# Optimization experiments

Hardware: AMD Instinct MI355X
Metric: run time of the kernel (lower is better)

## Reference

```python
import jax, jax.numpy as jnp
import numpy as np

D_EMB, D_PROJ, N_HEADS, HIDDEN = 640, 256, 4, 128
HEAD_DIM = D_PROJ // N_HEADS
B = 65536
EPS = 1e-5


def setup_inputs() -> dict:
    key = jax.random.key(0)
    ks = jax.random.split(key, 14)
    def w(k, shape, fan_in):
        return (jax.random.normal(k, shape, jnp.float32) / np.sqrt(fan_in)).astype(jnp.float32)
    return {
        "global_diff": jax.random.normal(ks[0], (B, D_EMB), jnp.float32),
        "local_diff": jax.random.normal(ks[1], (B, D_EMB), jnp.float32),
        # global/local projections ([in, out] layout; math identical to torch Linear)
        "Wg": w(ks[2], (D_EMB, D_PROJ), D_EMB), "bg": jnp.zeros((D_PROJ,), jnp.float32),
        "Wl": w(ks[3], (D_EMB, D_PROJ), D_EMB), "bl": jnp.zeros((D_PROJ,), jnp.float32),
        # MultiheadAttention packed in-proj (q|k|v) and out-proj
        "W_in": w(ks[4], (D_PROJ, 3 * D_PROJ), D_PROJ), "b_in": jnp.zeros((3 * D_PROJ,), jnp.float32),
        "W_out": w(ks[5], (D_PROJ, D_PROJ), D_PROJ), "b_out": jnp.zeros((D_PROJ,), jnp.float32),
        # LayerNorm
        "gamma": jnp.ones((D_PROJ,), jnp.float32), "beta": jnp.zeros((D_PROJ,), jnp.float32),
        # MLP head
        "W1": w(ks[6], (D_PROJ, HIDDEN), D_PROJ), "b1": jnp.zeros((HIDDEN,), jnp.float32),
        "W2": w(ks[7], (HIDDEN, 1), HIDDEN), "b2": jnp.zeros((1,), jnp.float32),
    }


def reference(global_diff, local_diff, Wg, bg, Wl, bl, W_in, b_in, W_out, b_out,
              gamma, beta, W1, b1, W2, b2):
    # projections (eval mode: dropout inactive)
    g = global_diff @ Wg + bg              # [B, P] -- the single query token
    l = local_diff @ Wl + bl               # [B, P]
    kv = jnp.stack([g, l], axis=1)         # [B, 2, P]

    Wq, Wk, Wv = jnp.split(W_in, 3, axis=1)
    bq, bk, bv = jnp.split(b_in, 3)
    b = g.shape[0]
    q = (g @ Wq + bq).reshape(b, N_HEADS, HEAD_DIM)        # [B, H, d]
    k = (kv @ Wk + bk).reshape(b, 2, N_HEADS, HEAD_DIM)    # [B, 2, H, d]
    v = (kv @ Wv + bv).reshape(b, 2, N_HEADS, HEAD_DIM)

    scale = 1.0 / np.sqrt(HEAD_DIM)
    scores = jnp.einsum('bhd,bshd->bhs', q, k) * scale     # [B, H, 2]
    attn = jax.nn.softmax(scores, axis=-1)
    ctx = jnp.einsum('bhs,bshd->bhd', attn, v).reshape(b, D_PROJ)
    attended = ctx @ W_out + b_out                         # [B, P]

    # residual + LayerNorm (eps=1e-5, torch default)
    x = g + attended
    mu = jnp.mean(x, axis=-1, keepdims=True)
    var = jnp.mean(jnp.square(x - mu), axis=-1, keepdims=True)
    y = (x - mu) * jax.lax.rsqrt(var + EPS) * gamma + beta

    # MLP head: Linear -> exact GELU (torch default) -> Linear
    h = jax.nn.gelu(y @ W1 + b1, approximate=False)
    out = (h @ W2 + b2).squeeze(-1)                        # [B]
    return out
```

## Files before the change

kernel.cpp:

```cpp
#include <hip/hip_runtime.h>
#include <math.h>

typedef __attribute__((ext_vector_type(4))) float f32x4;
typedef __attribute__((ext_vector_type(8))) __bf16 bf16x8;

static constexpr int WG_OFF = 0;
static constexpr int WL_OFF = 163840;
static constexpr int WQ_OFF = 327680;
static constexpr int WK_OFF = 393216;
static constexpr int WV_OFF = 458752;
static constexpr int WO_OFF = 524288;
static constexpr int W1_OFF = 589824;
static constexpr int W_TOTAL = 622592;

__device__ __forceinline__ unsigned short f2bf(float f) {
  unsigned u = __builtin_bit_cast(unsigned, f);
  u += 0x7FFFu + ((u >> 16) & 1u);
  return (unsigned short)(u >> 16);
}

__device__ __forceinline__ f32x4 mfma16(bf16x8 a, bf16x8 b, f32x4 c) {
  return __builtin_amdgcn_mfma_f32_16x16x32_bf16(a, b, c, 0, 0, 0);
}
__device__ __forceinline__ f32x4 fzero4() {
  f32x4 v; v[0] = 0.f; v[1] = 0.f; v[2] = 0.f; v[3] = 0.f; return v;
}

__device__ __forceinline__ bf16x8 ldB(const unsigned short* __restrict__ ws, int fragIdx, int lane) {
  return *(const bf16x8*)(ws + (size_t)(fragIdx * 64 + lane) * 8);
}

template <int STRIDE>
__device__ __forceinline__ bf16x8 ldA(const char* s, int row, int kbyte) {
  return *(const bf16x8*)(s + row * STRIDE + (kbyte ^ ((row & 7) << 4)));
}

__device__ __forceinline__ void stC(char* s, int row, int col, float v) {
  *(__bf16*)(s + row * 512 + ((col * 2) ^ ((row & 7) << 4))) = (__bf16)v;
}
__device__ __forceinline__ float ldC(const char* s, int row, int col) {
  return (float)*(const __bf16*)(s + row * 512 + ((col * 2) ^ ((row & 7) << 4)));
}

__device__ __forceinline__ bf16x8 cvt8(float4 a, float4 b) {
  bf16x8 t;
  t[0] = (__bf16)a.x; t[1] = (__bf16)a.y; t[2] = (__bf16)a.z; t[3] = (__bf16)a.w;
  t[4] = (__bf16)b.x; t[5] = (__bf16)b.y; t[6] = (__bf16)b.z; t[7] = (__bf16)b.w;
  return t;
}

template <int N>
__device__ __forceinline__ void red16(float* v) {
#pragma unroll
  for (int m = 1; m < 16; m <<= 1) {
#pragma unroll
    for (int i = 0; i < N; ++i) v[i] += __shfl_xor(v[i], m);
  }
}

__device__ __forceinline__ void stageA32(const float* __restrict__ A, char* sA, int tid) {
#pragma unroll
  for (int i = 0; i < 5; ++i) {
    const int idx = i * 512 + tid;
    const int row = idx / 80;
    const int c8 = idx - row * 80;
    const float* ap = A + (size_t)idx * 8;
    float4 f0 = *(const float4*)ap;
    float4 f1 = *(const float4*)(ap + 4);
    *(bf16x8*)(sA + row * 1280 + ((c8 * 16) ^ ((row & 7) << 4))) = cvt8(f0, f1);
  }
}

__device__ __forceinline__ void proj640(const char* sA, const unsigned short* __restrict__ wsW,
                                        const float* __restrict__ bias, char* sDst,
                                        int f0, int lane) {
  const int l15 = lane & 15, kg4 = lane >> 4;
  f32x4 acc[2][2];
#pragma unroll
  for (int m = 0; m < 2; ++m)
#pragma unroll
    for (int n = 0; n < 2; ++n) acc[m][n] = fzero4();
#pragma unroll 2
  for (int kt = 0; kt < 20; ++kt) {
    bf16x8 b0 = ldB(wsW, kt * 16 + f0, lane);
    bf16x8 b1 = ldB(wsW, kt * 16 + f0 + 1, lane);
    const int kb = kt * 64 + kg4 * 16;
#pragma unroll
    for (int m = 0; m < 2; ++m) {
      bf16x8 a = ldA<1280>(sA, m * 16 + l15, kb);
      acc[m][0] = mfma16(a, b0, acc[m][0]);
      acc[m][1] = mfma16(a, b1, acc[m][1]);
    }
  }
#pragma unroll
  for (int n = 0; n < 2; ++n) {
    const int col = (f0 + n) * 16 + l15;
    const float bv = bias[col];
#pragma unroll
    for (int m = 0; m < 2; ++m)
#pragma unroll
      for (int r = 0; r < 4; ++r)
        stC(sDst, m * 16 + kg4 * 4 + r, col, acc[m][n][r] + bv);
  }
}

__device__ __forceinline__ void gemm256(const char* sA, const unsigned short* __restrict__ wsW,
                                        int f0, f32x4 (&acc)[2][2], int lane) {
  const int l15 = lane & 15, kg4 = lane >> 4;
#pragma unroll 2
  for (int kt = 0; kt < 8; ++kt) {
    bf16x8 b0 = ldB(wsW, kt * 16 + f0, lane);
    bf16x8 b1 = ldB(wsW, kt * 16 + f0 + 1, lane);
    const int kb = kt * 64 + kg4 * 16;
#pragma unroll
    for (int m = 0; m < 2; ++m) {
      bf16x8 a = ldA<512>(sA, m * 16 + l15, kb);
      acc[m][0] = mfma16(a, b0, acc[m][0]);
      acc[m][1] = mfma16(a, b1, acc[m][1]);
    }
  }
}

__device__ __forceinline__ void gemm256d(const char* sG, const char* sL,
                                         const unsigned short* __restrict__ wsW, int f0,
                                         f32x4 (&ag)[2][2], f32x4 (&al)[2][2], int lane) {
  const int l15 = lane & 15, kg4 = lane >> 4;
#pragma unroll 2
  for (int kt = 0; kt < 8; ++kt) {
    bf16x8 b0 = ldB(wsW, kt * 16 + f0, lane);
    bf16x8 b1 = ldB(wsW, kt * 16 + f0 + 1, lane);
    const int kb = kt * 64 + kg4 * 16;
#pragma unroll
    for (int m = 0; m < 2; ++m) {
      bf16x8 g = ldA<512>(sG, m * 16 + l15, kb);
      bf16x8 l = ldA<512>(sL, m * 16 + l15, kb);
      ag[m][0] = mfma16(g, b0, ag[m][0]);
      ag[m][1] = mfma16(g, b1, ag[m][1]);
      al[m][0] = mfma16(l, b0, al[m][0]);
      al[m][1] = mfma16(l, b1, al[m][1]);
    }
  }
}

__global__ void convert_w(const float* __restrict__ Wg, const float* __restrict__ Wl,
                          const float* __restrict__ Win, const float* __restrict__ Wout,
                          const float* __restrict__ W1, unsigned short* __restrict__ ws) {
  const int tid = blockIdx.x * 256 + threadIdx.x;
  if (tid >= W_TOTAL) return;
  const float* src;
  int stride, coloff, base, lognf;
  if (tid < WL_OFF)      { src = Wg;   stride = 256; coloff = 0;   base = WG_OFF; lognf = 4; }
  else if (tid < WQ_OFF) { src = Wl;   stride = 256; coloff = 0;   base = WL_OFF; lognf = 4; }
  else if (tid < WK_OFF) { src = Win;  stride = 768; coloff = 0;   base = WQ_OFF; lognf = 4; }
  else if (tid < WV_OFF) { src = Win;  stride = 768; coloff = 256; base = WK_OFF; lognf = 4; }
  else if (tid < WO_OFF) { src = Win;  stride = 768; coloff = 512; base = WV_OFF; lognf = 4; }
  else if (tid < W1_OFF) { src = Wout; stride = 256; coloff = 0;   base = WO_OFF; lognf = 4; }
  else                   { src = W1;   stride = 128; coloff = 0;   base = W1_OFF; lognf = 3; }
  const int idx = tid - base;
  const int j = idx & 7;
  const int lane = (idx >> 3) & 63;
  const int fl = idx >> 9;
  const int n = fl & ((1 << lognf) - 1);
  const int kt = fl >> lognf;
  const int k = kt * 32 + (lane >> 4) * 8 + j;
  const int col = coloff + n * 16 + (lane & 15);
  ws[tid] = f2bf(src[k * stride + col]);
}

__global__ __launch_bounds__(512)
__attribute__((amdgpu_waves_per_eu(4, 4)))
void dca_fused(
    const float* __restrict__ gdiff, const float* __restrict__ ldiff,
    const float* __restrict__ bg, const float* __restrict__ bl,
    const float* __restrict__ bin, const float* __restrict__ bout,
    const float* __restrict__ gamma, const float* __restrict__ beta,
    const float* __restrict__ b1, const float* __restrict__ W2,
    const float* __restrict__ b2, const unsigned short* __restrict__ wsw,
    float* __restrict__ out) {
  __shared__ __align__(16) char sMem[73728];
  char* sA = sMem;
  char* sG = sMem + 40960;
  char* sL = sMem + 57344;
  float* sSc = (float*)sMem;
  float* sLN = (float*)(sMem + 2048);
  float* sMu = (float*)(sMem + 4096);
  float* sPO = (float*)(sMem + 4352);

  const int tid = threadIdx.x;
  const int blk = blockIdx.x;
  const int lane = tid & 63, l15 = lane & 15, kg4 = lane >> 4;
  const int w = tid >> 6;
  const int f0 = w * 2;

  stageA32(gdiff + (size_t)blk * 32 * 640, sA, tid);
  __syncthreads();
  proj640(sA, wsw + WG_OFF, bg, sG, f0, lane);
  __syncthreads();
  stageA32(ldiff + (size_t)blk * 32 * 640, sA, tid);
  __syncthreads();
  proj640(sA, wsw + WL_OFF, bl, sL, f0, lane);
  __syncthreads();

  f32x4 q[2][2], kg[2][2], kl[2][2];
#pragma unroll
  for (int m = 0; m < 2; ++m)
#pragma unroll
    for (int n = 0; n < 2; ++n) { q[m][n] = fzero4(); kg[m][n] = fzero4(); kl[m][n] = fzero4(); }
#pragma unroll 1
  for (int kt = 0; kt < 8; ++kt) {
    bf16x8 bq0 = ldB(wsw + WQ_OFF, kt * 16 + f0, lane);
    bf16x8 bq1 = ldB(wsw + WQ_OFF, kt * 16 + f0 + 1, lane);
    bf16x8 bk0 = ldB(wsw + WK_OFF, kt * 16 + f0, lane);
    bf16x8 bk1 = ldB(wsw + WK_OFF, kt * 16 + f0 + 1, lane);
    const int kb = kt * 64 + kg4 * 16;
#pragma unroll
    for (int m = 0; m < 2; ++m) {
      bf16x8 g = ldA<512>(sG, m * 16 + l15, kb);
      bf16x8 l = ldA<512>(sL, m * 16 + l15, kb);
      q[m][0] = mfma16(g, bq0, q[m][0]);
      q[m][1] = mfma16(g, bq1, q[m][1]);
      kg[m][0] = mfma16(g, bk0, kg[m][0]);
      kg[m][1] = mfma16(g, bk1, kg[m][1]);
      kl[m][0] = mfma16(l, bk0, kl[m][0]);
      kl[m][1] = mfma16(l, bk1, kl[m][1]);
    }
  }
  float s[16];
#pragma unroll
  for (int m = 0; m < 2; ++m) {
#pragma unroll
    for (int r = 0; r < 4; ++r) {
      float t0 = 0.f, t1 = 0.f;
#pragma unroll
      for (int n = 0; n < 2; ++n) {
        const float qv = q[m][n][r] + bin[(f0 + n) * 16 + l15];
        t0 += qv * kg[m][n][r];
        t1 += qv * kl[m][n][r];
      }
      s[m * 4 + r] = t0;
      s[8 + m * 4 + r] = t1;
    }
  }
  red16<16>(s);
  if (l15 < 2) {
#pragma unroll
    for (int r = 0; r < 4; ++r) {
      const int row = l15 * 16 + kg4 * 4 + r;
      sSc[(w * 32 + row) * 2 + 0] = s[l15 * 4 + r];
      sSc[(w * 32 + row) * 2 + 1] = s[8 + l15 * 4 + r];
    }
  }
  __syncthreads();
  float a1v[2][4];
  {
    const int pw = w ^ 1;
#pragma unroll
    for (int m = 0; m < 2; ++m)
#pragma unroll
      for (int r = 0; r < 4; ++r) {
        const int row = m * 16 + kg4 * 4 + r;
        const float t0 = s[m * 4 + r] + sSc[(pw * 32 + row) * 2 + 0];
        const float t1 = s[8 + m * 4 + r] + sSc[(pw * 32 + row) * 2 + 1];
        a1v[m][r] = 1.0f / (1.0f + expf((t0 - t1) * 0.125f));
      }
  }

  f32x4 ctx[2][2];
  {
    f32x4 vg[2][2], vl[2][2];
#pragma unroll
    for (int m = 0; m < 2; ++m) {
      vg[m][0] = fzero4(); vg[m][1] = fzero4();
      vl[m][0] = fzero4(); vl[m][1] = fzero4();
    }
    gemm256d(sG, sL, wsw + WV_OFF, f0, vg, vl, lane);
#pragma unroll
    for (int n = 0; n < 2; ++n) {
      const float bv = bin[512 + (f0 + n) * 16 + l15];
#pragma unroll
      for (int m = 0; m < 2; ++m)
#pragma unroll
        for (int r = 0; r < 4; ++r)
          ctx[m][n][r] = (1.0f - a1v[m][r]) * vg[m][n][r] + a1v[m][r] * vl[m][n][r] + bv;
    }
  }
  __syncthreads();
#pragma unroll
  for (int n = 0; n < 2; ++n) {
    const int col = (f0 + n) * 16 + l15;
#pragma unroll
    for (int m = 0; m < 2; ++m)
#pragma unroll
      for (int r = 0; r < 4; ++r)
        stC(sL, m * 16 + kg4 * 4 + r, col, ctx[m][n][r]);
  }
  __syncthreads();

  {
    f32x4 at[2][2];
#pragma unroll
    for (int m = 0; m < 2; ++m) { at[m][0] = fzero4(); at[m][1] = fzero4(); }
    gemm256(sL, wsw + WO_OFF, f0, at, lane);
    float st[16];
#pragma unroll
    for (int i = 0; i < 16; ++i) st[i] = 0.f;
#pragma unroll
    for (int n = 0; n < 2; ++n) {
      const int col = (f0 + n) * 16 + l15;
      const float bv = bout[col];
#pragma unroll
      for (int m = 0; m < 2; ++m)
#pragma unroll
        for (int r = 0; r < 4; ++r) {
          const int row = m * 16 + kg4 * 4 + r;
          const float x = at[m][n][r] + bv + ldC(sG, row, col);
          stC(sG, row, col, x);
          st[m * 4 + r] += x;
          st[8 + m * 4 + r] += x * x;
        }
    }
    red16<16>(st);
    if (l15 < 2) {
#pragma unroll
      for (int r = 0; r < 4; ++r) {
        const int row = l15 * 16 + kg4 * 4 + r;
        sLN[(w * 32 + row) * 2 + 0] = st[l15 * 4 + r];
        sLN[(w * 32 + row) * 2 + 1] = st[8 + l15 * 4 + r];
      }
    }
  }
  __syncthreads();
  if (tid < 64) {
    const int row = tid >> 1, j = tid & 1;
    float v = 0.f;
#pragma unroll
    for (int ww = 0; ww < 8; ++ww) v += sLN[(ww * 32 + row) * 2 + j];
    sMu[row * 2 + j] = v;
  }
  __syncthreads();
#pragma unroll
  for (int n = 0; n < 2; ++n) {
    const int col = (f0 + n) * 16 + l15;
    const float ga = gamma[col], be = beta[col];
#pragma unroll
    for (int m = 0; m < 2; ++m)
#pragma unroll
      for (int r = 0; r < 4; ++r) {
        const int row = m * 16 + kg4 * 4 + r;
        const float m_ = sMu[row * 2 + 0] * (1.0f / 256.0f);
        const float var = sMu[row * 2 + 1] * (1.0f / 256.0f) - m_ * m_;
        const float x = ldC(sG, row, col);
        stC(sG, row, col, (x - m_) * rsqrtf(var + 1e-5f) * ga + be);
      }
  }
  __syncthreads();

  f32x4 ha[2];
  ha[0] = fzero4();
  ha[1] = fzero4();
#pragma unroll 2
  for (int kt = 0; kt < 8; ++kt) {
    bf16x8 b = ldB(wsw + W1_OFF, kt * 8 + w, lane);
    const int kb = kt * 64 + kg4 * 16;
#pragma unroll
    for (int m = 0; m < 2; ++m) {
      bf16x8 a = ldA<512>(sG, m * 16 + l15, kb);
      ha[m] = mfma16(a, b, ha[m]);
    }
  }
  {
    const int colh = w * 16 + l15;
    const float bv1 = b1[colh], w2v = W2[colh];
    float o[8];
#pragma unroll
    for (int m = 0; m < 2; ++m)
#pragma unroll
      for (int r = 0; r < 4; ++r) {
        float hv = ha[m][r] + bv1;
        hv = 0.5f * hv * (1.0f + erff(hv * 0.70710678118654752f));
        o[m * 4 + r] = hv * w2v;
      }
    red16<8>(o);
    if (l15 < 2) {
#pragma unroll
      for (int r = 0; r < 4; ++r)
        sPO[w * 32 + l15 * 16 + kg4 * 4 + r] = o[l15 * 4 + r];
    }
  }
  __syncthreads();
  if (tid < 32) {
    float acc = b2[0];
#pragma unroll
    for (int ww = 0; ww < 8; ++ww) acc += sPO[ww * 32 + tid];
    out[(size_t)blk * 32 + tid] = acc;
  }
}

extern "C" void kernel_launch(void* const* d_in, const int* in_sizes, int n_in,
                              void* d_out, int out_size, void* d_ws, size_t ws_size,
                              hipStream_t stream) {
  (void)in_sizes; (void)n_in; (void)out_size; (void)ws_size;
  const float* gdiff = (const float*)d_in[0];
  const float* ldiff = (const float*)d_in[1];
  const float* Wg    = (const float*)d_in[2];
  const float* bg    = (const float*)d_in[3];
  const float* Wl    = (const float*)d_in[4];
  const float* bl    = (const float*)d_in[5];
  const float* Win   = (const float*)d_in[6];
  const float* bin   = (const float*)d_in[7];
  const float* Wout  = (const float*)d_in[8];
  const float* bout  = (const float*)d_in[9];
  const float* gamma = (const float*)d_in[10];
  const float* beta  = (const float*)d_in[11];
  const float* W1    = (const float*)d_in[12];
  const float* b1    = (const float*)d_in[13];
  const float* W2    = (const float*)d_in[14];
  const float* b2    = (const float*)d_in[15];
  unsigned short* ws = (unsigned short*)d_ws;
  float* out = (float*)d_out;

  convert_w<<<dim3((W_TOTAL + 255) / 256), dim3(256), 0, stream>>>(Wg, Wl, Win, Wout, W1, ws);
  dca_fused<<<dim3(2048), dim3(512), 0, stream>>>(gdiff, ldiff, bg, bl, bin, bout, gamma,
                                                  beta, b1, W2, b2,
                                                  (const unsigned short*)ws, out);
}
```

Measured before the change: 205.3 us.

## Double-buffer K-halves of input staging to overlap global loads with MFMA

Each 32x640 input tile is split into two 320-column halves held in two LDS buffers. Loading and converting the next half now runs alongside the MFMA projection of the current half, chaining across the global and local inputs. The goal is to hide global-memory latency that the old stage, sync, compute sequence exposed. The cost is a shorter k-loop per call and heavier register pressure from loads in flight, and the `#pragma unroll` on the staging loop is dropped.

```diff
diff --git a/kernel.cpp b/kernel.cpp
--- a/kernel.cpp
+++ b/kernel.cpp
@@ -58,40 +58,37 @@
   }
 }
 
-__device__ __forceinline__ void stageA32(const float* __restrict__ A, char* sA, int tid) {
-#pragma unroll
-  for (int i = 0; i < 5; ++i) {
-    const int idx = i * 512 + tid;
-    const int row = idx / 80;
-    const int c8 = idx - row * 80;
-    const float* ap = A + (size_t)idx * 8;
+__device__ __forceinline__ void stageHalf(const float* __restrict__ A, int half, char* sA, int tid) {
+  for (int c = tid; c < 1280; c += 512) {
+    const int row = c / 40;
+    const int c8 = c - row * 40;
+    const float* ap = A + (size_t)row * 640 + half * 320 + c8 * 8;
     float4 f0 = *(const float4*)ap;
     float4 f1 = *(const float4*)(ap + 4);
-    *(bf16x8*)(sA + row * 1280 + ((c8 * 16) ^ ((row & 7) << 4))) = cvt8(f0, f1);
-  }
-}
-
-__device__ __forceinline__ void proj640(const char* sA, const unsigned short* __restrict__ wsW,
-                                        const float* __restrict__ bias, char* sDst,
-                                        int f0, int lane) {
+    *(bf16x8*)(sA + row * 640 + ((c8 * 16) ^ ((row & 7) << 4))) = cvt8(f0, f1);
+  }
+}
+
+__device__ __forceinline__ void projHalf(const char* sA, const unsigned short* __restrict__ wsW,
+                                         int ktBase, f32x4 (&acc)[2][2], int f0, int lane) {
   const int l15 = lane & 15, kg4 = lane >> 4;
-  f32x4 acc[2][2];
-#pragma unroll
-  for (int m = 0; m < 2; ++m)
-#pragma unroll
-    for (int n = 0; n < 2; ++n) acc[m][n] = fzero4();
 #pragma unroll 2
-  for (int kt = 0; kt < 20; ++kt) {
-    bf16x8 b0 = ldB(wsW, kt * 16 + f0, lane);
-    bf16x8 b1 = ldB(wsW, kt * 16 + f0 + 1, lane);
+  for (int kt = 0; kt < 10; ++kt) {
+    bf16x8 b0 = ldB(wsW, (ktBase + kt) * 16 + f0, lane);
+    bf16x8 b1 = ldB(wsW, (ktBase + kt) * 16 + f0 + 1, lane);
     const int kb = kt * 64 + kg4 * 16;
 #pragma unroll
     for (int m = 0; m < 2; ++m) {
-      bf16x8 a = ldA<1280>(sA, m * 16 + l15, kb);
+      bf16x8 a = ldA<640>(sA, m * 16 + l15, kb);
       acc[m][0] = mfma16(a, b0, acc[m][0]);
       acc[m][1] = mfma16(a, b1, acc[m][1]);
     }
   }
+}
+
+__device__ __forceinline__ void writeTile(f32x4 (&acc)[2][2], const float* __restrict__ bias,
+                                          char* sDst, int f0, int lane) {
+  const int l15 = lane & 15, kg4 = lane >> 4;
 #pragma unroll
   for (int n = 0; n < 2; ++n) {
     const int col = (f0 + n) * 16 + l15;
@@ -178,7 +175,8 @@
     const float* __restrict__ b2, const unsigned short* __restrict__ wsw,
     float* __restrict__ out) {
   __shared__ __align__(16) char sMem[73728];
-  char* sA = sMem;
+  char* sA0 = sMem;
+  char* sA1 = sMem + 20480;
   char* sG = sMem + 40960;
   char* sL = sMem + 57344;
   float* sSc = (float*)sMem;
@@ -192,14 +190,31 @@
   const int w = tid >> 6;
   const int f0 = w * 2;
 
-  stageA32(gdiff + (size_t)blk * 32 * 640, sA, tid);
-  __syncthreads();
-  proj640(sA, wsw + WG_OFF, bg, sG, f0, lane);
-  __syncthreads();
-  stageA32(ldiff + (size_t)blk * 32 * 640, sA, tid);
-  __syncthreads();
-  proj640(sA, wsw + WL_OFF, bl, sL, f0, lane);
-  __syncthreads();
+  const float* Ag = gdiff + (size_t)blk * 32 * 640;
+  const float* Al = ldiff + (size_t)blk * 32 * 640;
+
+  {
+    f32x4 acc[2][2];
+#pragma unroll
+    for (int m = 0; m < 2; ++m) { acc[m][0] = fzero4(); acc[m][1] = fzero4(); }
+    stageHalf(Ag, 0, sA0, tid);
+    __syncthreads();
+    stageHalf(Ag, 1, sA1, tid);
+    projHalf(sA0, wsw + WG_OFF, 0, acc, f0, lane);
+    __syncthreads();
+    stageHalf(Al, 0, sA0, tid);
+    projHalf(sA1, wsw + WG_OFF, 10, acc, f0, lane);
+    writeTile(acc, bg, sG, f0, lane);
+    __syncthreads();
+#pragma unroll
+    for (int m = 0; m < 2; ++m) { acc[m][0] = fzero4(); acc[m][1] = fzero4(); }
+    stageHalf(Al, 1, sA1, tid);
+    projHalf(sA0, wsw + WL_OFF, 0, acc, f0, lane);
+    __syncthreads();
+    projHalf(sA1, wsw + WL_OFF, 10, acc, f0, lane);
+    writeTile(acc, bl, sL, f0, lane);
+    __syncthreads();
+  }
 
   f32x4 q[2][2], kg[2][2], kl[2][2];
 #pragma unroll
```

Result: slower. 210.3 us (+2.4%).
